# Kernel tuning notes

Measured on AMD Instinct MI355X. Metric: run time of the kernel, lower is better.

Reference implementation:

```python
import jax, jax.numpy as jnp
import numpy as np

B, T, C, H = 4, 2048, 768, 12
D = C // H  # head_size = 64
ROPE_BASE = 10000.0


def rotary_tables(seq_len, dim, dtype=jnp.float32):
    # dim = head_size; uses dim//2 frequencies
    inv_freq = 1.0 / (ROPE_BASE ** (jnp.arange(0, dim, 2, dtype=jnp.float32) / dim))
    t = jnp.arange(seq_len, dtype=jnp.float32)
    freqs = jnp.outer(t, inv_freq)  # [T, D/2]
    return jnp.cos(freqs).astype(dtype), jnp.sin(freqs).astype(dtype)


def apply_rotary(x, cos, sin):
    # x: [B, H, T, D]; cos/sin: [T, D/2] broadcast over B,H
    d = x.shape[-1] // 2
    x1, x2 = x[..., :d], x[..., d:]
    y1 = x1 * cos + x2 * sin
    y2 = -x1 * sin + x2 * cos
    return jnp.concatenate([y1, y2], axis=-1)


def setup_inputs() -> dict:
    key = jax.random.key(0)
    ks = jax.random.split(key, 5)
    x = jax.random.normal(ks[0], (B, T, C), dtype=jnp.float32)
    W_attn = jax.random.normal(ks[1], (C, 3 * C), dtype=jnp.float32) * (1.0 / np.sqrt(C))
    b_attn = jax.random.normal(ks[2], (3 * C,), dtype=jnp.float32) * 0.02
    W_proj = jax.random.normal(ks[3], (C, C), dtype=jnp.float32) * (1.0 / np.sqrt(C))
    b_proj = jax.random.normal(ks[4], (C,), dtype=jnp.float32) * 0.02
    return {"x": x, "W_attn": W_attn, "b_attn": b_attn, "W_proj": W_proj, "b_proj": b_proj}


def reference(x, W_attn, b_attn, W_proj, b_proj):
    Bx, Tx, Cx = x.shape
    qkv = x @ W_attn + b_attn  # [B, T, 3C]
    q, k, v = jnp.split(qkv, 3, axis=-1)
    # [B, T, C] -> [B, H, T, D]
    to_heads = lambda a: a.reshape(Bx, Tx, H, D).transpose(0, 2, 1, 3)
    q, k, v = to_heads(q), to_heads(k), to_heads(v)
    cos, sin = rotary_tables(Tx, D, x.dtype)
    q = apply_rotary(q, cos, sin)
    k = apply_rotary(k, cos, sin)
    scale = 1.0 / np.sqrt(D)
    scores = jnp.einsum('bhqd,bhkd->bhqk', q, k) * scale  # [B, H, T, T]
    causal = jnp.tril(jnp.ones((Tx, Tx), dtype=bool))
    scores = jnp.where(causal, scores, jnp.finfo(scores.dtype).min)
    attn = jax.nn.softmax(scores, axis=-1)
    y = jnp.einsum('bhqk,bhkd->bhqd', attn, v)  # [B, H, T, D]
    y = y.transpose(0, 2, 1, 3).reshape(Bx, Tx, Cx)
    return y @ W_proj + b_proj
```

## Files before the change

### kernel.cpp

```cpp
#include <hip/hip_runtime.h>
#include <hip/hip_bf16.h>

#define BB 4
#define TT 2048
#define CC 768
#define HH 12
#define DD 64
#define MM (BB * TT)
#define BH (BB * HH)

typedef __bf16 bf16_t;
typedef __bf16 bf16x8 __attribute__((ext_vector_type(8)));
typedef __bf16 bf16x4 __attribute__((ext_vector_type(4)));
typedef float f32x4 __attribute__((ext_vector_type(4)));

__device__ __forceinline__ float fast_exp2(float x) {
#if __has_builtin(__builtin_amdgcn_exp2f)
    return __builtin_amdgcn_exp2f(x);
#else
    return exp2f(x);
#endif
}

__device__ __forceinline__ uint32_t pk2(float lo, float hi) {
    bf16_t l = (bf16_t)lo, h = (bf16_t)hi;
    uint16_t lu = __builtin_bit_cast(uint16_t, l);
    uint16_t hu = __builtin_bit_cast(uint16_t, h);
    return ((uint32_t)hu << 16) | lu;
}

__device__ __forceinline__ void gload_lds16(const void* g, void* l) {
    __builtin_amdgcn_global_load_lds(
        (const __attribute__((address_space(1))) uint32_t*)g,
        (__attribute__((address_space(3))) uint32_t*)l, 16, 0, 0);
}

__global__ void cvt_f32_bf16(const float* __restrict__ in, bf16_t* __restrict__ out, int n4) {
    int tid = blockIdx.x * blockDim.x + threadIdx.x;
    if (tid >= n4) return;
    float4 v = ((const float4*)in)[tid];
    bf16x4 o;
    o[0] = (bf16_t)v.x; o[1] = (bf16_t)v.y; o[2] = (bf16_t)v.z; o[3] = (bf16_t)v.w;
    ((bf16x4*)out)[tid] = o;
}

__global__ void transpose_cvt(const float* __restrict__ W, bf16_t* __restrict__ WT, int K, int N) {
    __shared__ bf16_t tile[32][33];
    int k0 = blockIdx.x * 32, n0 = blockIdx.y * 32;
    int tx = threadIdx.x, ty = threadIdx.y;
#pragma unroll
    for (int r = 0; r < 4; ++r) {
        int kl = ty * 4 + r;
        tile[kl][tx] = (bf16_t)W[(size_t)(k0 + kl) * N + n0 + tx];
    }
    __syncthreads();
#pragma unroll
    for (int r = 0; r < 4; ++r) {
        int nl = ty * 4 + r;
        WT[(size_t)(n0 + nl) * K + k0 + tx] = tile[tx][nl];
    }
}

template <bool OUT_BF16>
__global__ __launch_bounds__(256, 3) void gemm_bias(
        const bf16_t* __restrict__ A, const bf16_t* __restrict__ BT,
        const float* __restrict__ bias, void* __restrict__ Cout, int N) {
    const int K = 768;
    __shared__ bf16_t As[2][128 * 32];
    __shared__ bf16_t Bs[2][128 * 32];
    int tid = threadIdx.x;
    int wv = tid >> 6, lane = tid & 63, c = lane & 15, quad = lane >> 4;
    int wm = (wv >> 1) * 64, wn = (wv & 1) * 64;
    int m0 = blockIdx.x * 128, n0 = blockIdx.y * 128;

    int srow = wv * 32 + (lane >> 2);
    int slot = lane & 3;

    auto stage = [&](int buf, int k0) {
#pragma unroll
        for (int ins = 0; ins < 2; ++ins) {
            int r = srow + ins * 16;
            int g = (slot - ((r >> 1) & 3)) & 3;
            const bf16_t* ga = A + (size_t)(m0 + r) * K + k0 + g * 8;
            const bf16_t* gb = BT + (size_t)(n0 + r) * K + k0 + g * 8;
            gload_lds16(ga, &As[buf][(wv * 32 + ins * 16) * 32]);
            gload_lds16(gb, &Bs[buf][(wv * 32 + ins * 16) * 32]);
        }
    };

    f32x4 acc[4][4] = {};
    int s_rd = (quad + ((c >> 1) & 3)) & 3;

    const int nk = K / 32;
    stage(0, 0);
    for (int kt = 0; kt < nk; ++kt) {
        __syncthreads();
        if (kt + 1 < nk) stage((kt + 1) & 1, (kt + 1) * 32);
        int buf = kt & 1;
        bf16x8 af[4], bfr[4];
#pragma unroll
        for (int i = 0; i < 4; ++i) af[i] = *(const bf16x8*)&As[buf][(wm + i * 16 + c) * 32 + s_rd * 8];
#pragma unroll
        for (int j = 0; j < 4; ++j) bfr[j] = *(const bf16x8*)&Bs[buf][(wn + j * 16 + c) * 32 + s_rd * 8];
#pragma unroll
        for (int i = 0; i < 4; ++i)
#pragma unroll
            for (int j = 0; j < 4; ++j)
                acc[i][j] = __builtin_amdgcn_mfma_f32_16x16x32_bf16(af[i], bfr[j], acc[i][j], 0, 0, 0);
    }
#pragma unroll
    for (int j = 0; j < 4; ++j) {
        int col = n0 + wn + j * 16 + c;
        float bv = bias[col];
#pragma unroll
        for (int i = 0; i < 4; ++i) {
            int row = m0 + wm + i * 16 + quad * 4;
#pragma unroll
            for (int r = 0; r < 4; ++r) {
                float v = acc[i][j][r] + bv;
                if (OUT_BF16) ((bf16_t*)Cout)[(size_t)(row + r) * N + col] = (bf16_t)v;
                else          ((float*)Cout)[(size_t)(row + r) * N + col] = v;
            }
        }
    }
}

__global__ void rotary_qk(const bf16_t* __restrict__ qkv, bf16_t* __restrict__ Q, bf16_t* __restrict__ Kc) {
    int tid = blockIdx.x * blockDim.x + threadIdx.x;
    int i = tid & 31;
    int rem = tid >> 5;
    int h = rem % HH;
    int row = rem / HH;
    int b = row >> 11, t = row & (TT - 1);
    const bf16_t* base = qkv + (size_t)row * (3 * CC) + h * DD + i;
    float q1 = (float)base[0],  q2 = (float)base[32];
    float k1 = (float)base[CC], k2 = (float)base[CC + 32];
    float inv = powf(10000.0f, -(float)i * (1.0f / 32.0f));
    float fr = (float)t * inv;
    float cs = cosf(fr), sn = sinf(fr);
    const float scale = 0.125f * 1.44269504088896f;
    size_t o = ((size_t)(b * HH + h) * TT + t) * DD + i;
    Q[o]      = (bf16_t)((q1 * cs + q2 * sn) * scale);
    Q[o + 32] = (bf16_t)((-q1 * sn + q2 * cs) * scale);
    Kc[o]      = (bf16_t)(k1 * cs + k2 * sn);
    Kc[o + 32] = (bf16_t)(-k1 * sn + k2 * cs);
}

__global__ void vtrans(const bf16_t* __restrict__ qkv, bf16_t* __restrict__ Vt) {
    int bh = blockIdx.x;
    int kt = blockIdx.y;
    int t0 = kt * 64;
    int b = bh / HH, h = bh % HH;
    __shared__ bf16_t tile[64][66];
    int tx = threadIdx.x & 63, ty = threadIdx.x >> 6;
#pragma unroll
    for (int r = 0; r < 16; ++r) {
        int tl = ty * 16 + r;
        tile[tl][tx] = qkv[(size_t)(b * TT + t0 + tl) * (3 * CC) + 2 * CC + h * DD + tx];
    }
    __syncthreads();
#pragma unroll
    for (int r = 0; r < 16; ++r) {
        int dl = ty * 16 + r;
        Vt[(((size_t)bh * (TT / 64) + kt) * 64 + dl) * 64 + tx] = tile[tx][dl];
    }
}

__global__ __launch_bounds__(256, 3) void flash_attn(
        const bf16_t* __restrict__ Q, const bf16_t* __restrict__ Kc,
        const bf16_t* __restrict__ Vt, bf16_t* __restrict__ Y) {
    __shared__ bf16_t Ks[2][64 * 64];
    __shared__ bf16_t Vs[2][64 * 64];
    int blk = blockIdx.x;
    int qt = 15 - blk / BH;
    int bh = blk % BH;
    int wv = threadIdx.x >> 6, lane = threadIdx.x & 63;
    int b = bh / HH, h = bh - b * HH;
    int c = lane & 15, quad = lane >> 4;
    int qb0 = qt * 128, qbw = qb0 + wv * 32;
    const bf16_t* Qg = Q + ((size_t)bh * TT + qbw) * DD;
    const bf16_t* Kg = Kc + (size_t)bh * TT * DD;
    const bf16_t* Vg = Vt + (size_t)bh * (TT / 64) * 64 * 64;

    bf16x8 qf[2][2];
#pragma unroll
    for (int s = 0; s < 2; ++s)
#pragma unroll
        for (int ch = 0; ch < 2; ++ch)
            qf[s][ch] = *(const bf16x8*)(Qg + (s * 16 + c) * DD + ch * 32 + quad * 8);

    int srow = wv * 16 + (lane >> 3);
    int slot = lane & 7;
    auto stage = [&](int buf, int kt64) {
#pragma unroll
        for (int ins = 0; ins < 2; ++ins) {
            int r = srow + ins * 8;
            int g = (slot - (r & 7)) & 7;
            gload_lds16(Kg + (size_t)(kt64 * 64 + r) * 64 + g * 8, &Ks[buf][(wv * 16 + ins * 8) * 64]);
            gload_lds16(Vg + (size_t)kt64 * 4096 + r * 64 + g * 8, &Vs[buf][(wv * 16 + ins * 8) * 64]);
        }
    };

    f32x4 O[2][4] = {};
    float lsum[2] = {0.0f, 0.0f};
    int lane_lo = c + ((quad & 1) << 5);
    int lane_hi = lane_lo + 16;
    bool lowq = (quad < 2);

    int ntiles = 2 * qt + 2;
    stage(0, 0);
    for (int kt = 0; kt < ntiles; ++kt) {
        __syncthreads();
        if (kt + 1 < ntiles) stage((kt + 1) & 1, kt + 1);
        int buf = kt & 1;
#pragma unroll
        for (int t32 = 0; t32 < 2; ++t32) {
            int ks = kt * 64 + t32 * 32;
            if (ks > qbw) continue;
            bool masked = (ks == qbw);
            bf16x8 kf[2][2], vf[4];
#pragma unroll
            for (int t2 = 0; t2 < 2; ++t2)
#pragma unroll
                for (int ch = 0; ch < 2; ++ch) {
                    int row = t32 * 32 + t2 * 16 + c;
                    int sl = (ch * 4 + quad + (c & 7)) & 7;
                    kf[t2][ch] = *(const bf16x8*)&Ks[buf][row * 64 + sl * 8];
                }
#pragma unroll
            for (int nt = 0; nt < 4; ++nt) {
                int row = nt * 16 + c;
                int sl = (t32 * 4 + quad + (c & 7)) & 7;
                vf[nt] = *(const bf16x8*)&Vs[buf][row * 64 + sl * 8];
            }
            f32x4 st[2][2] = {};
#pragma unroll
            for (int s = 0; s < 2; ++s)
#pragma unroll
                for (int t2 = 0; t2 < 2; ++t2) {
                    st[s][t2] = __builtin_amdgcn_mfma_f32_16x16x32_bf16(kf[t2][0], qf[s][0], st[s][t2], 0, 0, 0);
                    st[s][t2] = __builtin_amdgcn_mfma_f32_16x16x32_bf16(kf[t2][1], qf[s][1], st[s][t2], 0, 0, 0);
                }
#pragma unroll
            for (int s = 0; s < 2; ++s) {
                float pv[2][4];
#pragma unroll
                for (int t2 = 0; t2 < 2; ++t2)
#pragma unroll
                    for (int r = 0; r < 4; ++r) {
                        float p = fast_exp2(st[s][t2][r]);
                        if (masked) {
                            int keyl = t2 * 16 + quad * 4 + r;
                            if (keyl > s * 16 + c) p = 0.0f;
                        }
                        pv[t2][r] = p;
                    }
                lsum[s] += ((pv[0][0] + pv[0][1]) + (pv[0][2] + pv[0][3]))
                         + ((pv[1][0] + pv[1][1]) + (pv[1][2] + pv[1][3]));
                uint32_t pk0a = pk2(pv[0][0], pv[0][1]), pk0b = pk2(pv[0][2], pv[0][3]);
                uint32_t pk1a = pk2(pv[1][0], pv[1][1]), pk1b = pk2(pv[1][2], pv[1][3]);
                union { uint32_t u[4]; bf16x8 v; } pf;
                {
                    uint32_t x0 = (uint32_t)__shfl((int)pk0a, lane_lo);
                    uint32_t y0 = (uint32_t)__shfl((int)pk1a, lane_lo);
                    pf.u[0] = lowq ? x0 : y0;
                    uint32_t x1 = (uint32_t)__shfl((int)pk0b, lane_lo);
                    uint32_t y1 = (uint32_t)__shfl((int)pk1b, lane_lo);
                    pf.u[1] = lowq ? x1 : y1;
                    uint32_t x2 = (uint32_t)__shfl((int)pk0a, lane_hi);
                    uint32_t y2 = (uint32_t)__shfl((int)pk1a, lane_hi);
                    pf.u[2] = lowq ? x2 : y2;
                    uint32_t x3 = (uint32_t)__shfl((int)pk0b, lane_hi);
                    uint32_t y3 = (uint32_t)__shfl((int)pk1b, lane_hi);
                    pf.u[3] = lowq ? x3 : y3;
                }
#pragma unroll
                for (int nt = 0; nt < 4; ++nt)
                    O[s][nt] = __builtin_amdgcn_mfma_f32_16x16x32_bf16(vf[nt], pf.v, O[s][nt], 0, 0, 0);
            }
        }
    }

#pragma unroll
    for (int s = 0; s < 2; ++s) {
        float l = lsum[s];
        l += __shfl_xor(l, 16);
        l += __shfl_xor(l, 32);
        float inv_l = 1.0f / l;
        int row = b * TT + qbw + s * 16 + c;
#pragma unroll
        for (int nt = 0; nt < 4; ++nt) {
            bf16x4 ov;
#pragma unroll
            for (int r = 0; r < 4; ++r) ov[r] = (bf16_t)(O[s][nt][r] * inv_l);
            *(bf16x4*)(Y + (size_t)row * CC + h * DD + nt * 16 + quad * 4) = ov;
        }
    }
}

extern "C" void kernel_launch(void* const* d_in, const int* in_sizes, int n_in,
                              void* d_out, int out_size, void* d_ws, size_t ws_size,
                              hipStream_t stream) {
    const float* x      = (const float*)d_in[0];
    const float* W_attn = (const float*)d_in[1];
    const float* b_attn = (const float*)d_in[2];
    const float* W_proj = (const float*)d_in[3];
    const float* b_proj = (const float*)d_in[4];
    float* out = (float*)d_out;

    unsigned char* ws = (unsigned char*)d_ws;
    size_t off = 0;
    auto alloc = [&](size_t bytes) { void* p = ws + off; off += (bytes + 255) & ~(size_t)255; return p; };
    bf16_t* xb  = (bf16_t*)alloc((size_t)MM * CC * 2);
    bf16_t* WaT = (bf16_t*)alloc((size_t)3 * CC * CC * 2);
    bf16_t* WpT = (bf16_t*)alloc((size_t)CC * CC * 2);
    bf16_t* qkv = (bf16_t*)alloc((size_t)MM * 3 * CC * 2);
    bf16_t* Qh  = (bf16_t*)alloc((size_t)BH * TT * DD * 2);
    bf16_t* Kh  = (bf16_t*)alloc((size_t)BH * TT * DD * 2);
    bf16_t* Vt  = (bf16_t*)alloc((size_t)BH * TT * DD * 2);
    bf16_t* Yb  = (bf16_t*)alloc((size_t)MM * CC * 2);

    cvt_f32_bf16<<<(MM * CC / 4 + 255) / 256, 256, 0, stream>>>(x, xb, MM * CC / 4);
    transpose_cvt<<<dim3(CC / 32, 3 * CC / 32), dim3(32, 8), 0, stream>>>(W_attn, WaT, CC, 3 * CC);
    transpose_cvt<<<dim3(CC / 32, CC / 32), dim3(32, 8), 0, stream>>>(W_proj, WpT, CC, CC);
    gemm_bias<true><<<dim3(MM / 128, 3 * CC / 128), 256, 0, stream>>>(xb, WaT, b_attn, qkv, 3 * CC);
    rotary_qk<<<(MM * HH * 32) / 256, 256, 0, stream>>>(qkv, Qh, Kh);
    vtrans<<<dim3(BH, TT / 64), 256, 0, stream>>>(qkv, Vt);
    flash_attn<<<dim3(768), 256, 0, stream>>>(Qh, Kh, Vt, Yb);
    gemm_bias<false><<<dim3(MM / 128, CC / 128), 256, 0, stream>>>(Yb, WpT, b_proj, out, CC);
}
```

Measured before the change: 223.9 us.

## Fuse rotary embedding and V transpose into QKV GEMM epilogue

The QKV GEMM epilogue now applies bias, rotary embedding and the softmax scale directly, writing head-major Q and K and a tiled transposed V. This removes the separate rotary and V-transpose kernels and the round trip through the intermediate qkv buffer. In exchange, the epilogue runs per-element cosf/sinf/powf inside the GEMM, which raises register pressure, and the Q/K stores are scattered 2-byte writes.

```diff
diff --git a/kernel.cpp b/kernel.cpp
--- a/kernel.cpp
+++ b/kernel.cpp
@@ -61,53 +61,105 @@
     }
 }
 
-template <bool OUT_BF16>
-__global__ __launch_bounds__(256, 3) void gemm_bias(
+#define GEMM_CORE(A_, BT_, acc_)                                                       \
+    __shared__ bf16_t As[2][128 * 32];                                                 \
+    __shared__ bf16_t Bs[2][128 * 32];                                                 \
+    int tid = threadIdx.x;                                                             \
+    int wv = tid >> 6, lane = tid & 63, c = lane & 15, quad = lane >> 4;               \
+    int wm = (wv >> 1) * 64, wn = (wv & 1) * 64;                                       \
+    int m0 = blockIdx.x * 128, n0 = blockIdx.y * 128;                                  \
+    int srow = wv * 32 + (lane >> 2);                                                  \
+    int slot = lane & 3;                                                               \
+    auto stage = [&](int buf, int k0) {                                                \
+        _Pragma("unroll")                                                              \
+        for (int ins = 0; ins < 2; ++ins) {                                            \
+            int r = srow + ins * 16;                                                   \
+            int g = (slot - ((r >> 1) & 3)) & 3;                                       \
+            const bf16_t* ga = A_ + (size_t)(m0 + r) * K + k0 + g * 8;                 \
+            const bf16_t* gb = BT_ + (size_t)(n0 + r) * K + k0 + g * 8;                \
+            gload_lds16(ga, &As[buf][(wv * 32 + ins * 16) * 32]);                      \
+            gload_lds16(gb, &Bs[buf][(wv * 32 + ins * 16) * 32]);                      \
+        }                                                                              \
+    };                                                                                 \
+    int s_rd = (quad + ((c >> 1) & 3)) & 3;                                            \
+    const int nk = K / 32;                                                             \
+    stage(0, 0);                                                                       \
+    for (int kt = 0; kt < nk; ++kt) {                                                  \
+        __syncthreads();                                                               \
+        if (kt + 1 < nk) stage((kt + 1) & 1, (kt + 1) * 32);                           \
+        int buf = kt & 1;                                                              \
+        bf16x8 af[4], bfr[4];                                                          \
+        _Pragma("unroll")                                                              \
+        for (int i = 0; i < 4; ++i) af[i] = *(const bf16x8*)&As[buf][(wm + i * 16 + c) * 32 + s_rd * 8];  \
+        _Pragma("unroll")                                                              \
+        for (int j = 0; j < 4; ++j) bfr[j] = *(const bf16x8*)&Bs[buf][(wn + j * 16 + c) * 32 + s_rd * 8]; \
+        _Pragma("unroll")                                                              \
+        for (int i = 0; i < 4; ++i)                                                    \
+            _Pragma("unroll")                                                          \
+            for (int j = 0; j < 4; ++j)                                                \
+                acc_[i][j] = __builtin_amdgcn_mfma_f32_16x16x32_bf16(af[i], bfr[j], acc_[i][j], 0, 0, 0); \
+    }
+
+__global__ __launch_bounds__(256, 3) void gemm_qkv(
         const bf16_t* __restrict__ A, const bf16_t* __restrict__ BT,
-        const float* __restrict__ bias, void* __restrict__ Cout, int N) {
+        const float* __restrict__ bias,
+        bf16_t* __restrict__ Qh, bf16_t* __restrict__ Kh, bf16_t* __restrict__ Vt) {
     const int K = 768;
-    __shared__ bf16_t As[2][128 * 32];
-    __shared__ bf16_t Bs[2][128 * 32];
-    int tid = threadIdx.x;
-    int wv = tid >> 6, lane = tid & 63, c = lane & 15, quad = lane >> 4;
-    int wm = (wv >> 1) * 64, wn = (wv & 1) * 64;
-    int m0 = blockIdx.x * 128, n0 = blockIdx.y * 128;
-
-    int srow = wv * 32 + (lane >> 2);
-    int slot = lane & 3;
-
-    auto stage = [&](int buf, int k0) {
-#pragma unroll
-        for (int ins = 0; ins < 2; ++ins) {
-            int r = srow + ins * 16;
-            int g = (slot - ((r >> 1) & 3)) & 3;
-            const bf16_t* ga = A + (size_t)(m0 + r) * K + k0 + g * 8;
-            const bf16_t* gb = BT + (size_t)(n0 + r) * K + k0 + g * 8;
-            gload_lds16(ga, &As[buf][(wv * 32 + ins * 16) * 32]);
-            gload_lds16(gb, &Bs[buf][(wv * 32 + ins * 16) * 32]);
-        }
-    };
-
     f32x4 acc[4][4] = {};
-    int s_rd = (quad + ((c >> 1) & 3)) & 3;
-
-    const int nk = K / 32;
-    stage(0, 0);
-    for (int kt = 0; kt < nk; ++kt) {
-        __syncthreads();
-        if (kt + 1 < nk) stage((kt + 1) & 1, (kt + 1) * 32);
-        int buf = kt & 1;
-        bf16x8 af[4], bfr[4];
-#pragma unroll
-        for (int i = 0; i < 4; ++i) af[i] = *(const bf16x8*)&As[buf][(wm + i * 16 + c) * 32 + s_rd * 8];
-#pragma unroll
-        for (int j = 0; j < 4; ++j) bfr[j] = *(const bf16x8*)&Bs[buf][(wn + j * 16 + c) * 32 + s_rd * 8];
-#pragma unroll
-        for (int i = 0; i < 4; ++i)
-#pragma unroll
-            for (int j = 0; j < 4; ++j)
-                acc[i][j] = __builtin_amdgcn_mfma_f32_16x16x32_bf16(af[i], bfr[j], acc[i][j], 0, 0, 0);
-    }
+    GEMM_CORE(A, BT, acc)
+
+    int type = n0 / 768;
+    int hloc = ((n0 % 768) + wn) >> 6;
+    int bidx = m0 >> 11;
+    int colb = n0 + wn;
+
+    if (type < 2) {
+        const float rscale = (type == 0) ? 0.125f * 1.44269504088896f : 1.0f;
+        bf16_t* dst = (type == 0 ? Qh : Kh) + ((size_t)(bidx * HH + hloc) * TT) * DD;
+#pragma unroll
+        for (int j = 0; j < 2; ++j) {
+            int dlo = j * 16 + c;
+            float infr = powf(10000.0f, -(float)dlo * (1.0f / 32.0f));
+            float blo = bias[colb + j * 16 + c];
+            float bhi = bias[colb + (j + 2) * 16 + c];
+#pragma unroll
+            for (int i = 0; i < 4; ++i)
+#pragma unroll
+                for (int r = 0; r < 4; ++r) {
+                    int t = (m0 + wm + i * 16 + quad * 4 + r) & (TT - 1);
+                    float a = acc[i][j][r] + blo;
+                    float b2 = acc[i][j + 2][r] + bhi;
+                    float fr = (float)t * infr;
+                    float cs = cosf(fr), sn = sinf(fr);
+                    dst[(size_t)t * DD + dlo]      = (bf16_t)((a * cs + b2 * sn) * rscale);
+                    dst[(size_t)t * DD + dlo + 32] = (bf16_t)((-a * sn + b2 * cs) * rscale);
+                }
+        }
+    } else {
+        bf16_t* dstV = Vt + (size_t)(bidx * HH + hloc) * (TT / 64) * 4096;
+#pragma unroll
+        for (int j = 0; j < 4; ++j) {
+            int dim = j * 16 + c;
+            float bv = bias[colb + j * 16 + c];
+#pragma unroll
+            for (int i = 0; i < 4; ++i) {
+                int tbase = (m0 + wm + i * 16 + quad * 4) & (TT - 1);
+                int kt64 = tbase >> 6, tin = tbase & 63;
+                bf16x4 ov;
+#pragma unroll
+                for (int r = 0; r < 4; ++r) ov[r] = (bf16_t)(acc[i][j][r] + bv);
+                *(bf16x4*)&dstV[((size_t)kt64 * 64 + dim) * 64 + tin] = ov;
+            }
+        }
+    }
+}
+
+__global__ __launch_bounds__(256, 3) void gemm_proj(
+        const bf16_t* __restrict__ A, const bf16_t* __restrict__ BT,
+        const float* __restrict__ bias, float* __restrict__ Cout) {
+    const int K = 768;
+    f32x4 acc[4][4] = {};
+    GEMM_CORE(A, BT, acc)
 #pragma unroll
     for (int j = 0; j < 4; ++j) {
         int col = n0 + wn + j * 16 + c;
@@ -116,53 +168,9 @@
         for (int i = 0; i < 4; ++i) {
             int row = m0 + wm + i * 16 + quad * 4;
 #pragma unroll
-            for (int r = 0; r < 4; ++r) {
-                float v = acc[i][j][r] + bv;
-                if (OUT_BF16) ((bf16_t*)Cout)[(size_t)(row + r) * N + col] = (bf16_t)v;
-                else          ((float*)Cout)[(size_t)(row + r) * N + col] = v;
-            }
-        }
-    }
-}
-
-__global__ void rotary_qk(const bf16_t* __restrict__ qkv, bf16_t* __restrict__ Q, bf16_t* __restrict__ Kc) {
-    int tid = blockIdx.x * blockDim.x + threadIdx.x;
-    int i = tid & 31;
-    int rem = tid >> 5;
-    int h = rem % HH;
-    int row = rem / HH;
-    int b = row >> 11, t = row & (TT - 1);
-    const bf16_t* base = qkv + (size_t)row * (3 * CC) + h * DD + i;
-    float q1 = (float)base[0],  q2 = (float)base[32];
-    float k1 = (float)base[CC], k2 = (float)base[CC + 32];
-    float inv = powf(10000.0f, -(float)i * (1.0f / 32.0f));
-    float fr = (float)t * inv;
-    float cs = cosf(fr), sn = sinf(fr);
-    const float scale = 0.125f * 1.44269504088896f;
-    size_t o = ((size_t)(b * HH + h) * TT + t) * DD + i;
-    Q[o]      = (bf16_t)((q1 * cs + q2 * sn) * scale);
-    Q[o + 32] = (bf16_t)((-q1 * sn + q2 * cs) * scale);
-    Kc[o]      = (bf16_t)(k1 * cs + k2 * sn);
-    Kc[o + 32] = (bf16_t)(-k1 * sn + k2 * cs);
-}
-
-__global__ void vtrans(const bf16_t* __restrict__ qkv, bf16_t* __restrict__ Vt) {
-    int bh = blockIdx.x;
-    int kt = blockIdx.y;
-    int t0 = kt * 64;
-    int b = bh / HH, h = bh % HH;
-    __shared__ bf16_t tile[64][66];
-    int tx = threadIdx.x & 63, ty = threadIdx.x >> 6;
-#pragma unroll
-    for (int r = 0; r < 16; ++r) {
-        int tl = ty * 16 + r;
-        tile[tl][tx] = qkv[(size_t)(b * TT + t0 + tl) * (3 * CC) + 2 * CC + h * DD + tx];
-    }
-    __syncthreads();
-#pragma unroll
-    for (int r = 0; r < 16; ++r) {
-        int dl = ty * 16 + r;
-        Vt[(((size_t)bh * (TT / 64) + kt) * 64 + dl) * 64 + tx] = tile[tx][dl];
+            for (int r = 0; r < 4; ++r)
+                Cout[(size_t)(row + r) * CC + col] = acc[i][j][r] + bv;
+        }
     }
 }
 
@@ -177,10 +185,10 @@
     int wv = threadIdx.x >> 6, lane = threadIdx.x & 63;
     int b = bh / HH, h = bh - b * HH;
     int c = lane & 15, quad = lane >> 4;
-    int qb0 = qt * 128, qbw = qb0 + wv * 32;
+    int qbw = qt * 128 + wv * 32;
     const bf16_t* Qg = Q + ((size_t)bh * TT + qbw) * DD;
     const bf16_t* Kg = Kc + (size_t)bh * TT * DD;
-    const bf16_t* Vg = Vt + (size_t)bh * (TT / 64) * 64 * 64;
+    const bf16_t* Vg = Vt + (size_t)bh * (TT / 64) * 4096;
 
     bf16x8 qf[2][2];
 #pragma unroll
@@ -314,7 +322,6 @@
     bf16_t* xb  = (bf16_t*)alloc((size_t)MM * CC * 2);
     bf16_t* WaT = (bf16_t*)alloc((size_t)3 * CC * CC * 2);
     bf16_t* WpT = (bf16_t*)alloc((size_t)CC * CC * 2);
-    bf16_t* qkv = (bf16_t*)alloc((size_t)MM * 3 * CC * 2);
     bf16_t* Qh  = (bf16_t*)alloc((size_t)BH * TT * DD * 2);
     bf16_t* Kh  = (bf16_t*)alloc((size_t)BH * TT * DD * 2);
     bf16_t* Vt  = (bf16_t*)alloc((size_t)BH * TT * DD * 2);
@@ -323,9 +330,7 @@
     cvt_f32_bf16<<<(MM * CC / 4 + 255) / 256, 256, 0, stream>>>(x, xb, MM * CC / 4);
     transpose_cvt<<<dim3(CC / 32, 3 * CC / 32), dim3(32, 8), 0, stream>>>(W_attn, WaT, CC, 3 * CC);
     transpose_cvt<<<dim3(CC / 32, CC / 32), dim3(32, 8), 0, stream>>>(W_proj, WpT, CC, CC);
-    gemm_bias<true><<<dim3(MM / 128, 3 * CC / 128), 256, 0, stream>>>(xb, WaT, b_attn, qkv, 3 * CC);
-    rotary_qk<<<(MM * HH * 32) / 256, 256, 0, stream>>>(qkv, Qh, Kh);
-    vtrans<<<dim3(BH, TT / 64), 256, 0, stream>>>(qkv, Vt);
+    gemm_qkv<<<dim3(MM / 128, 3 * CC / 128), 256, 0, stream>>>(xb, WaT, b_attn, Qh, Kh, Vt);
     flash_attn<<<dim3(768), 256, 0, stream>>>(Qh, Kh, Vt, Yb);
-    gemm_bias<false><<<dim3(MM / 128, CC / 128), 256, 0, stream>>>(Yb, WpT, b_proj, out, CC);
-}
+    gemm_proj<<<dim3(MM / 128, CC / 128), 256, 0, stream>>>(Yb, WpT, b_proj, out);
+}
```

Measured after the change: 696.1 us. 3.11x slower.
